# Optimization experiments

Hardware: AMD Instinct MI355X
Metric: run time of the kernel (lower is better)

## Reference

```python
import jax, jax.numpy as jnp
import numpy as np

EMBED_DIM = 1024
NUM_HEADS = 16
HEAD_DIM = EMBED_DIM // NUM_HEADS
N, S = 4, 8192


def setup_inputs() -> dict:
    key = jax.random.key(0)
    ks = jax.random.split(key, 9)
    sc = 1.0 / np.sqrt(EMBED_DIM)
    d = {"x": jax.random.normal(ks[0], (N, S, EMBED_DIM), dtype=jnp.float32)}
    for i, name in enumerate(["Wq", "Wk", "Wv", "Wo"]):
        d[name] = jax.random.normal(ks[1 + i], (EMBED_DIM, EMBED_DIM), dtype=jnp.float32) * sc
    for i, name in enumerate(["bq", "bk", "bv", "bo"]):
        d[name] = jax.random.normal(ks[5 + i], (EMBED_DIM,), dtype=jnp.float32) * 0.01
    return d


def reference(x, Wq, Wk, Wv, Wo, bq, bk, bv, bo):
    n, s, e = x.shape
    # projections: nn.Linear => x @ W.T + b
    Q = x @ Wq.T + bq
    K = x @ Wk.T + bk
    V = x @ Wv.T + bv
    # (N, S, H, D) -> (N, H, S, D), matching torch .view().transpose(1, 2)
    Q = Q.reshape(n, s, NUM_HEADS, HEAD_DIM).transpose(0, 2, 1, 3)
    K = K.reshape(n, s, NUM_HEADS, HEAD_DIM).transpose(0, 2, 1, 3)
    V = V.reshape(n, s, NUM_HEADS, HEAD_DIM).transpose(0, 2, 1, 3)
    # Faithful to the original (buggy) einsum labeling: on (N,H,S,D) tensors
    # 'nqhd,nkhd->nhqk' attends OVER THE HEAD AXIS -> energy (N, S, H, H)
    energy = jnp.einsum('nqhd,nkhd->nhqk', Q, K)
    attention = jax.nn.softmax(energy / jnp.sqrt(jnp.float32(e)), axis=3)
    # out: (N, H, S, D), then reshaped as if (N, S, H*D) — exact original math
    out = jnp.einsum('nhql,nlhd->nqhd', attention, V).reshape(n, s, e)
    return out @ Wo.T + bo
```

## Files before the change

### kernel.cpp

```cpp
#include <hip/hip_runtime.h>
#include <cstdint>
#include <cstddef>

typedef unsigned short u16;
typedef __attribute__((ext_vector_type(8))) __bf16 bf16x8;
typedef __attribute__((ext_vector_type(4))) float floatx4;

typedef const __attribute__((address_space(1))) void* gptr_t;
typedef __attribute__((address_space(3))) void* lptr_t;

__device__ __forceinline__ u16 f2b(float f) {
    unsigned u = __builtin_bit_cast(unsigned, f);
    u += 0x7fffu + ((u >> 16) & 1u);
    return (u16)(u >> 16);
}

template <int N>
__device__ __forceinline__ float ror_add(float x) {
    int y = __builtin_amdgcn_update_dpp(0, __builtin_bit_cast(int, x), 0x120 + N, 0xF, 0xF, true);
    return x + __builtin_bit_cast(float, y);
}
template <int N>
__device__ __forceinline__ float ror_max(float x) {
    int y = __builtin_amdgcn_update_dpp(0, __builtin_bit_cast(int, x), 0x120 + N, 0xF, 0xF, true);
    return fmaxf(x, __builtin_bit_cast(float, y));
}

__global__ void cast_x(const float* __restrict__ in, u16* __restrict__ out, int n4) {
    const int stride = gridDim.x * blockDim.x;
    for (int i = blockIdx.x * blockDim.x + threadIdx.x; i < n4; i += stride) {
        const float4 v = ((const float4*)in)[i];
        ushort4 o;
        o.x = f2b(v.x); o.y = f2b(v.y); o.z = f2b(v.z); o.w = f2b(v.w);
        ((ushort4*)out)[i] = o;
    }
}

__global__ void cast_w(const float* __restrict__ Wq, const float* __restrict__ Wk,
                       const float* __restrict__ Wv, const float* __restrict__ Wo,
                       u16* __restrict__ Wqkv, u16* __restrict__ Wob) {
    const int stride = gridDim.x * blockDim.x;
    for (int i = blockIdx.x * blockDim.x + threadIdx.x; i < 1048576; i += stride) {
        const int which = i >> 18;
        const int local = i & 0x3FFFF;
        const float* src = which == 0 ? Wq : which == 1 ? Wk : which == 2 ? Wv : Wo;
        const float4 v = ((const float4*)src)[local];
        ushort4 o;
        o.x = f2b(v.x); o.y = f2b(v.y); o.z = f2b(v.z); o.w = f2b(v.w);
        ushort4* dst = which < 3 ? (ushort4*)Wqkv + which * 262144 + local
                                 : (ushort4*)Wob + local;
        *dst = o;
    }
}


#define MFMA16(va, vb, vc) __builtin_amdgcn_mfma_f32_16x16x32_bf16((va), (vb), (vc), 0, 0, 0)
#define PH_BAR()  __builtin_amdgcn_s_barrier()
#define PH_LGKM() asm volatile("s_waitcnt lgkmcnt(0)" ::: "memory")

template <bool OUT_BF16>
__global__ __launch_bounds__(512, 2)
void gemm8(const u16* __restrict__ A, const u16* __restrict__ B,
           const float* __restrict__ b0, const float* __restrict__ b1,
           const float* __restrict__ b2, void* __restrict__ Cout,
           int N, int mshift)
{
    __shared__ __align__(16) u16 lds[65536];

    const int nwg = gridDim.x;
    const int bid = blockIdx.x;
    const int swz = (bid & 7) * (nwg >> 3) + (bid >> 3);
    const int ntile = swz >> mshift;
    const int mtile = swz & ((1 << mshift) - 1);
    const int bm0 = mtile << 8;
    const int bn0 = ntile << 8;

    const int tid  = threadIdx.x;
    const int lane = tid & 63;
    const int wv   = tid >> 6;
    const int wm   = wv >> 2;
    const int wn   = wv & 3;
    const int lrow = lane & 15;
    const int quad = lane >> 4;

    const int srow = lane >> 2;
    const int scol = ((lane & 3) * 8) ^ (((lane >> 5) & 1) << 4);
    const u16* aS = A + (size_t)(bm0 + wv * 16 + srow) * 1024 + scol;
    const u16* bS = B + (size_t)(bn0 + wv * 16 + srow) * 1024 + scol;
    u16* aD = lds +         wv * 1024 + lane * 8;
    u16* bD = lds + 32768 + wv * 1024 + lane * 8;

    const int laneSw = lrow * 32 + ((quad * 8) ^ ((lrow >> 3) << 4));
    const u16* pA = lds +         wm * 8192 + laneSw;
    const u16* pB = lds + 32768 + wn * 4096 + laneSw;

    auto stage = [&](const u16* src, u16* dst, int kt, int half, int buf) {
        const u16* s = src + (size_t)half * 131072 + kt * 64;
        u16* d = dst + buf * 16384 + half * 8192;
        __builtin_amdgcn_global_load_lds((gptr_t)s,        (lptr_t)d,         16, 0, 0);
        __builtin_amdgcn_global_load_lds((gptr_t)(s + 32), (lptr_t)(d + 512), 16, 0, 0);
    };

    stage(aS, aD, 0, 0, 0);
    stage(aS, aD, 0, 1, 0);
    stage(bS, bD, 0, 0, 0);
    stage(bS, bD, 0, 1, 0);
    asm volatile("" ::: "memory");
    stage(bS, bD, 1, 0, 1);
    stage(bS, bD, 1, 1, 1);
    asm volatile("s_waitcnt vmcnt(4)" ::: "memory");
    PH_BAR();

    const floatx4 fz = {0.f, 0.f, 0.f, 0.f};
    floatx4 acc[8][4];
    #pragma unroll
    for (int i = 0; i < 8; ++i)
        #pragma unroll
        for (int t = 0; t < 4; ++t) acc[i][t] = fz;

    bf16x8 a[4][2], p0[2][2], p1[2][2];

    for (int j = 0; j < 8; ++j) {
        const int kt1 = 2 * j + 1;
        const int kt2 = 2 * j + 2;
        const int kt3 = 2 * j + 3;
        const bool more = (j < 7);

        #pragma unroll
        for (int i = 0; i < 4; ++i) {
            a[i][0] = *(const bf16x8*)(pA + i * 1024);
            a[i][1] = *(const bf16x8*)(pA + i * 1024 + 512);
        }
        #pragma unroll
        for (int t = 0; t < 2; ++t) {
            p0[t][0] = *(const bf16x8*)(pB + t * 1024);
            p0[t][1] = *(const bf16x8*)(pB + t * 1024 + 512);
        }
        stage(aS, aD, kt1, 0, 1);
        PH_BAR(); PH_LGKM();
        __builtin_amdgcn_s_setprio(1);
        #pragma unroll
        for (int i = 0; i < 4; ++i)
            #pragma unroll
            for (int t = 0; t < 2; ++t) {
                acc[i][t] = MFMA16(a[i][0], p0[t][0], acc[i][t]);
                acc[i][t] = MFMA16(a[i][1], p0[t][1], acc[i][t]);
            }
        __builtin_amdgcn_s_setprio(0);
        PH_BAR();

        #pragma unroll
        for (int t = 0; t < 2; ++t) {
            p1[t][0] = *(const bf16x8*)(pB + 2048 + t * 1024);
            p1[t][1] = *(const bf16x8*)(pB + 2048 + t * 1024 + 512);
        }
        stage(aS, aD, kt1, 1, 1);
        PH_BAR(); PH_LGKM();
        __builtin_amdgcn_s_setprio(1);
        #pragma unroll
        for (int i = 0; i < 4; ++i)
            #pragma unroll
            for (int t = 0; t < 2; ++t) {
                acc[i][2 + t] = MFMA16(a[i][0], p1[t][0], acc[i][2 + t]);
                acc[i][2 + t] = MFMA16(a[i][1], p1[t][1], acc[i][2 + t]);
            }
        __builtin_amdgcn_s_setprio(0);
        PH_BAR();

        #pragma unroll
        for (int i = 0; i < 4; ++i) {
            a[i][0] = *(const bf16x8*)(pA + 4096 + i * 1024);
            a[i][1] = *(const bf16x8*)(pA + 4096 + i * 1024 + 512);
        }
        if (more) stage(bS, bD, kt2, 0, 0);
        PH_BAR(); PH_LGKM();
        __builtin_amdgcn_s_setprio(1);
        #pragma unroll
        for (int i = 0; i < 4; ++i)
            #pragma unroll
            for (int t = 0; t < 2; ++t) {
                acc[4 + i][2 + t] = MFMA16(a[i][0], p1[t][0], acc[4 + i][2 + t]);
                acc[4 + i][2 + t] = MFMA16(a[i][1], p1[t][1], acc[4 + i][2 + t]);
            }
        __builtin_amdgcn_s_setprio(0);
        PH_BAR();

        if (more) stage(bS, bD, kt2, 1, 0);
        PH_BAR();
        __builtin_amdgcn_s_setprio(1);
        #pragma unroll
        for (int i = 0; i < 4; ++i)
            #pragma unroll
            for (int t = 0; t < 2; ++t) {
                acc[4 + i][t] = MFMA16(a[i][0], p0[t][0], acc[4 + i][t]);
                acc[4 + i][t] = MFMA16(a[i][1], p0[t][1], acc[4 + i][t]);
            }
        __builtin_amdgcn_s_setprio(0);
        if (more) asm volatile("s_waitcnt vmcnt(4)" ::: "memory");
        else      asm volatile("s_waitcnt vmcnt(0)" ::: "memory");
        PH_BAR();

        #pragma unroll
        for (int i = 0; i < 4; ++i) {
            a[i][0] = *(const bf16x8*)(pA + 16384 + i * 1024);
            a[i][1] = *(const bf16x8*)(pA + 16384 + i * 1024 + 512);
        }
        #pragma unroll
        for (int t = 0; t < 2; ++t) {
            p0[t][0] = *(const bf16x8*)(pB + 16384 + t * 1024);
            p0[t][1] = *(const bf16x8*)(pB + 16384 + t * 1024 + 512);
        }
        if (more) stage(aS, aD, kt2, 0, 0);
        PH_BAR(); PH_LGKM();
        __builtin_amdgcn_s_setprio(1);
        #pragma unroll
        for (int i = 0; i < 4; ++i)
            #pragma unroll
            for (int t = 0; t < 2; ++t) {
                acc[i][t] = MFMA16(a[i][0], p0[t][0], acc[i][t]);
                acc[i][t] = MFMA16(a[i][1], p0[t][1], acc[i][t]);
            }
        __builtin_amdgcn_s_setprio(0);
        PH_BAR();

        #pragma unroll
        for (int t = 0; t < 2; ++t) {
            p1[t][0] = *(const bf16x8*)(pB + 16384 + 2048 + t * 1024);
            p1[t][1] = *(const bf16x8*)(pB + 16384 + 2048 + t * 1024 + 512);
        }
        if (more) stage(aS, aD, kt2, 1, 0);
        PH_BAR(); PH_LGKM();
        __builtin_amdgcn_s_setprio(1);
        #pragma unroll
        for (int i = 0; i < 4; ++i)
            #pragma unroll
            for (int t = 0; t < 2; ++t) {
                acc[i][2 + t] = MFMA16(a[i][0], p1[t][0], acc[i][2 + t]);
                acc[i][2 + t] = MFMA16(a[i][1], p1[t][1], acc[i][2 + t]);
            }
        __builtin_amdgcn_s_setprio(0);
        PH_BAR();

        #pragma unroll
        for (int i = 0; i < 4; ++i) {
            a[i][0] = *(const bf16x8*)(pA + 16384 + 4096 + i * 1024);
            a[i][1] = *(const bf16x8*)(pA + 16384 + 4096 + i * 1024 + 512);
        }
        if (more) stage(bS, bD, kt3, 0, 1);
        PH_BAR(); PH_LGKM();
        __builtin_amdgcn_s_setprio(1);
        #pragma unroll
        for (int i = 0; i < 4; ++i)
            #pragma unroll
            for (int t = 0; t < 2; ++t) {
                acc[4 + i][2 + t] = MFMA16(a[i][0], p1[t][0], acc[4 + i][2 + t]);
                acc[4 + i][2 + t] = MFMA16(a[i][1], p1[t][1], acc[4 + i][2 + t]);
            }
        __builtin_amdgcn_s_setprio(0);
        PH_BAR();

        if (more) stage(bS, bD, kt3, 1, 1);
        PH_BAR();
        __builtin_amdgcn_s_setprio(1);
        #pragma unroll
        for (int i = 0; i < 4; ++i)
            #pragma unroll
            for (int t = 0; t < 2; ++t) {
                acc[4 + i][t] = MFMA16(a[i][0], p0[t][0], acc[4 + i][t]);
                acc[4 + i][t] = MFMA16(a[i][1], p0[t][1], acc[4 + i][t]);
            }
        __builtin_amdgcn_s_setprio(0);
        asm volatile("s_waitcnt vmcnt(4)" ::: "memory");
        PH_BAR();
    }

    float bsv[4];
    #pragma unroll
    for (int t = 0; t < 4; ++t) {
        const int n = bn0 + wn * 64 + t * 16 + lrow;
        const float* bp = n < 1024 ? b0 : (n < 2048 ? b1 : b2);
        bsv[t] = bp[n & 1023];
    }
    #pragma unroll
    for (int i = 0; i < 8; ++i) {
        const int mbase = bm0 + wm * 128 + i * 16 + quad * 4;
        #pragma unroll
        for (int t = 0; t < 4; ++t) {
            const int n = bn0 + wn * 64 + t * 16 + lrow;
            #pragma unroll
            for (int r = 0; r < 4; ++r) {
                const float v = acc[i][t][r] + bsv[t];
                const size_t idx = (size_t)(mbase + r) * N + n;
                if constexpr (OUT_BF16) ((u16*)Cout)[idx] = f2b(v);
                else                    ((float*)Cout)[idx] = v;
            }
        }
    }
}

__global__ __launch_bounds__(256)
void attn_v3(const u16* __restrict__ QKV, u16* __restrict__ Z)
{
    __shared__ __align__(16) u16 sV[4][1024];
    __shared__ __align__(16) u16 sA[4][640];
    __shared__ __align__(16) u16 sY[16 * 1152];

    const int tid  = threadIdx.x;
    const int lane = tid & 63;
    const int wv   = tid >> 6;
    const int lrow = lane & 15;
    const int quad = lane >> 4;
    const int pp   = lane >> 3;
    const int cc   = lane & 7;

    #pragma unroll
    for (int i = 0; i < 4; i++) {
        const int idx = i * 64 + lane;
        sA[wv][(idx >> 4) * 40 + 16 + (idx & 15)] = 0;
    }

    const int tgrp = blockIdx.x * 16;
    const int nb   = tgrp >> 13;
    const int sg   = (tgrp & 8191) >> 4;

    const floatx4 fzero = {0.f, 0.f, 0.f, 0.f};

    for (int tt = 0; tt < 4; tt++) {
        const int t = wv * 4 + tt;
        const u16* base = QKV + (size_t)(tgrp + t) * 3072;

        const bf16x8 q0 = *(const bf16x8*)(base + lrow * 64      + quad * 8);
        const bf16x8 q1 = *(const bf16x8*)(base + lrow * 64 + 32 + quad * 8);
        const bf16x8 k0 = *(const bf16x8*)(base + 1024 + lrow * 64      + quad * 8);
        const bf16x8 k1 = *(const bf16x8*)(base + 1024 + lrow * 64 + 32 + quad * 8);

        const u16* V = base + 2048;
        const bf16x8 va = *(const bf16x8*)(V + (2 * pp)     * 64 + cc * 8);
        const bf16x8 vb = *(const bf16x8*)(V + (2 * pp + 1) * 64 + cc * 8);
        #pragma unroll
        for (int s = 0; s < 8; s++) {
            const unsigned pv = (unsigned)__builtin_bit_cast(u16, (__bf16)va[s]) |
                                ((unsigned)__builtin_bit_cast(u16, (__bf16)vb[s]) << 16);
            *(unsigned*)&sV[wv][(s * 8 + cc) * 16 + 2 * pp] = pv;
        }

        floatx4 e = fzero;
        e = __builtin_amdgcn_mfma_f32_16x16x32_bf16(q0, k0, e, 0, 0, 0);
        e = __builtin_amdgcn_mfma_f32_16x16x32_bf16(q1, k1, e, 0, 0, 0);

        #pragma unroll
        for (int r = 0; r < 4; r++) {
            const float xv = e[r] * 0.03125f;
            float mx = xv;
            mx = ror_max<1>(mx); mx = ror_max<2>(mx);
            mx = ror_max<4>(mx); mx = ror_max<8>(mx);
            const float p = __expf(xv - mx);
            float s = p;
            s = ror_add<1>(s); s = ror_add<2>(s);
            s = ror_add<4>(s); s = ror_add<8>(s);
            sA[wv][(quad * 4 + r) * 40 + lrow] = f2b(p * __builtin_amdgcn_rcpf(s));
        }

        const bf16x8 af = *(const bf16x8*)&sA[wv][lrow * 40 + quad * 8];

        bf16x8 bfr[4];
        #pragma unroll
        for (int j = 0; j < 4; j++)
            #pragma unroll
            for (int jj = 0; jj < 8; jj++)
                bfr[j][jj] = __builtin_bit_cast(__bf16, (u16)0);
        if (quad < 2) {
            #pragma unroll
            for (int j = 0; j < 4; j++) {
                const int pr = (lrow & 7) * 8 + j * 2 + (lrow >> 3);
                bfr[j] = *(const bf16x8*)&sV[wv][pr * 16 + quad * 8];
            }
        }

        #pragma unroll
        for (int j = 0; j < 4; j++) {
            const floatx4 y = __builtin_amdgcn_mfma_f32_16x16x32_bf16(af, bfr[j], fzero, 0, 0, 0);
            #pragma unroll
            for (int r = 0; r < 4; r++)
                sY[t * 1152 + (quad * 4 + r) * 72 + j * 16 + lrow] = f2b(y[r]);
        }
    }

    __syncthreads();

    const int h   = tid >> 4;
    const int pos = tid & 15;
    u16* zrow = Z + (size_t)(nb * 8192 + h * 512 + sg) * 1024;
    #pragma unroll
    for (int it = 0; it < 8; it++) {
        const int c16 = it * 16 + pos;
        const int t = c16 >> 3, dc = c16 & 7;
        const uint4 v = *(const uint4*)&sY[t * 1152 + h * 72 + dc * 8];
        *(uint4*)(zrow + c16 * 8) = v;
    }
}

extern "C" void kernel_launch(void* const* d_in, const int* in_sizes, int n_in,
                              void* d_out, int out_size, void* d_ws, size_t ws_size,
                              hipStream_t stream)
{
    (void)in_sizes; (void)n_in; (void)out_size;
    const float* x  = (const float*)d_in[0];
    const float* Wq = (const float*)d_in[1];
    const float* Wk = (const float*)d_in[2];
    const float* Wv = (const float*)d_in[3];
    const float* Wo = (const float*)d_in[4];
    const float* bq = (const float*)d_in[5];
    const float* bk = (const float*)d_in[6];
    const float* bv = (const float*)d_in[7];
    const float* bo = (const float*)d_in[8];

    const size_t Mtot = 32768;
    char* ws = (char*)d_ws;
    u16* Xbf  = (u16*)ws;
    u16* Wqkv = (u16*)(ws + (64ull << 20));
    u16* Wob  = (u16*)(ws + (64ull << 20) + (6ull << 20));
    char* dyn = ws + (72ull << 20);
    const size_t fixed = (72ull << 20);

    int c = 4;
    for (int cc = 1; cc <= 4; cc <<= 1) {
        size_t Rr = Mtot / cc;
        if (fixed + Rr * 3072 * 2 + Rr * 1024 * 2 <= ws_size) { c = cc; break; }
    }
    const size_t R = Mtot / c;
    u16* QKV = (u16*)dyn;
    u16* Zb  = (u16*)(dyn + R * 3072 * 2);

    cast_x<<<dim3(4096), dim3(256), 0, stream>>>(x, Xbf, (int)(Mtot * 1024 / 4));
    cast_w<<<dim3(1024), dim3(256), 0, stream>>>(Wq, Wk, Wv, Wo, Wqkv, Wob);

    const int mt  = (int)(R >> 8);
    const int msh = __builtin_ctz((unsigned)mt);

    for (int ci = 0; ci < c; ci++) {
        const u16* Ab   = Xbf + (size_t)ci * R * 1024;
        float*     outp = (float*)d_out + (size_t)ci * R * 1024;
        gemm8<true><<<dim3(mt * 12), dim3(512), 0, stream>>>(Ab, Wqkv, bq, bk, bv, QKV, 3072, msh);
        attn_v3<<<dim3((unsigned)(R / 16)), dim3(256), 0, stream>>>(QKV, Zb);
        gemm8<false><<<dim3(mt * 4), dim3(512), 0, stream>>>(Zb, Wob, bo, bo, bo, outp, 1024, msh);
    }
}
```

Before: 573.3 us.

## Restructure GEMM main loop with double-buffered register fragments and sched barriers

Rewrites the bf16 GEMM inner loop so LDS fragment reads for the next MFMA block are issued before the current block's MFMAs, using separate even/odd register sets. It drops the explicit lgkmcnt(0) waits, stages whole A/B k-tiles at once, and adds sched_barrier fences with vmcnt waits at new points. The aim is to hide LDS read latency and cut barrier stalls between MFMA phases, at the cost of more VGPR pressure. Correctness now depends on the reworked buffer and wait-count accounting.

```diff
diff --git a/kernel.cpp b/kernel.cpp
--- a/kernel.cpp
+++ b/kernel.cpp
@@ -56,7 +56,19 @@
 
 #define MFMA16(va, vb, vc) __builtin_amdgcn_mfma_f32_16x16x32_bf16((va), (vb), (vc), 0, 0, 0)
 #define PH_BAR()  __builtin_amdgcn_s_barrier()
-#define PH_LGKM() asm volatile("s_waitcnt lgkmcnt(0)" ::: "memory")
+#define SB0()     __builtin_amdgcn_sched_barrier(0)
+#define VM4()     asm volatile("s_waitcnt vmcnt(4)" ::: "memory")
+#define VM0()     asm volatile("s_waitcnt vmcnt(0)" ::: "memory")
+
+#define MMA_BLK(af, bf, MI, TJ)                                                        \
+    _Pragma("unroll")                                                                  \
+    for (int i_ = 0; i_ < 4; ++i_) {                                                   \
+        _Pragma("unroll")                                                              \
+        for (int t_ = 0; t_ < 2; ++t_) {                                               \
+            acc[(MI)+i_][(TJ)+t_] = MFMA16(af[i_][0], bf[t_][0], acc[(MI)+i_][(TJ)+t_]); \
+            acc[(MI)+i_][(TJ)+t_] = MFMA16(af[i_][1], bf[t_][1], acc[(MI)+i_][(TJ)+t_]); \
+        }                                                                              \
+    }
 
 template <bool OUT_BF16>
 __global__ __launch_bounds__(512, 2)
@@ -94,22 +106,40 @@
     const u16* pA = lds +         wm * 8192 + laneSw;
     const u16* pB = lds + 32768 + wn * 4096 + laneSw;
 
-    auto stage = [&](const u16* src, u16* dst, int kt, int half, int buf) {
-        const u16* s = src + (size_t)half * 131072 + kt * 64;
-        u16* d = dst + buf * 16384 + half * 8192;
-        __builtin_amdgcn_global_load_lds((gptr_t)s,        (lptr_t)d,         16, 0, 0);
-        __builtin_amdgcn_global_load_lds((gptr_t)(s + 32), (lptr_t)(d + 512), 16, 0, 0);
+    auto stage2 = [&](const u16* src, u16* dst, int kt) {
+        #pragma unroll
+        for (int h = 0; h < 2; ++h) {
+            const u16* s = src + (size_t)h * 131072 + kt * 64;
+            u16* d = dst + h * 8192;
+            __builtin_amdgcn_global_load_lds((gptr_t)s,        (lptr_t)d,         16, 0, 0);
+            __builtin_amdgcn_global_load_lds((gptr_t)(s + 32), (lptr_t)(d + 512), 16, 0, 0);
+        }
     };
 
-    stage(aS, aD, 0, 0, 0);
-    stage(aS, aD, 0, 1, 0);
-    stage(bS, bD, 0, 0, 0);
-    stage(bS, bD, 0, 1, 0);
+    bf16x8 aE[4][2], aO[4][2], p1[2][2], p0E[2][2], p0O[2][2];
+
+    auto readA = [&](bf16x8 (&d)[4][2], int off) {
+        #pragma unroll
+        for (int i = 0; i < 4; ++i) {
+            d[i][0] = *(const bf16x8*)(pA + off + i * 1024);
+            d[i][1] = *(const bf16x8*)(pA + off + i * 1024 + 512);
+        }
+    };
+    auto readB = [&](bf16x8 (&d)[2][2], int off) {
+        #pragma unroll
+        for (int t = 0; t < 2; ++t) {
+            d[t][0] = *(const bf16x8*)(pB + off + t * 1024);
+            d[t][1] = *(const bf16x8*)(pB + off + t * 1024 + 512);
+        }
+    };
+
+    stage2(bS, bD, 0);
+    stage2(aS, aD, 0);
     asm volatile("" ::: "memory");
-    stage(bS, bD, 1, 0, 1);
-    stage(bS, bD, 1, 1, 1);
-    asm volatile("s_waitcnt vmcnt(4)" ::: "memory");
-    PH_BAR();
+    stage2(bS, bD + 16384, 1);
+    stage2(aS, aD + 16384, 1);
+    asm volatile("s_waitcnt vmcnt(8)" ::: "memory");
+    PH_BAR(); SB0();
 
     const floatx4 fz = {0.f, 0.f, 0.f, 0.f};
     floatx4 acc[8][4];
@@ -118,160 +148,81 @@
         #pragma unroll
         for (int t = 0; t < 4; ++t) acc[i][t] = fz;
 
-    bf16x8 a[4][2], p0[2][2], p1[2][2];
+    readA(aE, 0);
+    readB(p0E, 0);
 
     for (int j = 0; j < 8; ++j) {
-        const int kt1 = 2 * j + 1;
+        const bool more = (j < 7);
         const int kt2 = 2 * j + 2;
         const int kt3 = 2 * j + 3;
-        const bool more = (j < 7);
-
-        #pragma unroll
-        for (int i = 0; i < 4; ++i) {
-            a[i][0] = *(const bf16x8*)(pA + i * 1024);
-            a[i][1] = *(const bf16x8*)(pA + i * 1024 + 512);
-        }
-        #pragma unroll
-        for (int t = 0; t < 2; ++t) {
-            p0[t][0] = *(const bf16x8*)(pB + t * 1024);
-            p0[t][1] = *(const bf16x8*)(pB + t * 1024 + 512);
-        }
-        stage(aS, aD, kt1, 0, 1);
-        PH_BAR(); PH_LGKM();
-        __builtin_amdgcn_s_setprio(1);
-        #pragma unroll
-        for (int i = 0; i < 4; ++i)
-            #pragma unroll
-            for (int t = 0; t < 2; ++t) {
-                acc[i][t] = MFMA16(a[i][0], p0[t][0], acc[i][t]);
-                acc[i][t] = MFMA16(a[i][1], p0[t][1], acc[i][t]);
-            }
-        __builtin_amdgcn_s_setprio(0);
-        PH_BAR();
-
-        #pragma unroll
-        for (int t = 0; t < 2; ++t) {
-            p1[t][0] = *(const bf16x8*)(pB + 2048 + t * 1024);
-            p1[t][1] = *(const bf16x8*)(pB + 2048 + t * 1024 + 512);
-        }
-        stage(aS, aD, kt1, 1, 1);
-        PH_BAR(); PH_LGKM();
-        __builtin_amdgcn_s_setprio(1);
-        #pragma unroll
-        for (int i = 0; i < 4; ++i)
-            #pragma unroll
-            for (int t = 0; t < 2; ++t) {
-                acc[i][2 + t] = MFMA16(a[i][0], p1[t][0], acc[i][2 + t]);
-                acc[i][2 + t] = MFMA16(a[i][1], p1[t][1], acc[i][2 + t]);
-            }
-        __builtin_amdgcn_s_setprio(0);
-        PH_BAR();
-
-        #pragma unroll
-        for (int i = 0; i < 4; ++i) {
-            a[i][0] = *(const bf16x8*)(pA + 4096 + i * 1024);
-            a[i][1] = *(const bf16x8*)(pA + 4096 + i * 1024 + 512);
-        }
-        if (more) stage(bS, bD, kt2, 0, 0);
-        PH_BAR(); PH_LGKM();
-        __builtin_amdgcn_s_setprio(1);
-        #pragma unroll
-        for (int i = 0; i < 4; ++i)
-            #pragma unroll
-            for (int t = 0; t < 2; ++t) {
-                acc[4 + i][2 + t] = MFMA16(a[i][0], p1[t][0], acc[4 + i][2 + t]);
-                acc[4 + i][2 + t] = MFMA16(a[i][1], p1[t][1], acc[4 + i][2 + t]);
-            }
-        __builtin_amdgcn_s_setprio(0);
-        PH_BAR();
-
-        if (more) stage(bS, bD, kt2, 1, 0);
-        PH_BAR();
-        __builtin_amdgcn_s_setprio(1);
-        #pragma unroll
-        for (int i = 0; i < 4; ++i)
-            #pragma unroll
-            for (int t = 0; t < 2; ++t) {
-                acc[4 + i][t] = MFMA16(a[i][0], p0[t][0], acc[4 + i][t]);
-                acc[4 + i][t] = MFMA16(a[i][1], p0[t][1], acc[4 + i][t]);
-            }
-        __builtin_amdgcn_s_setprio(0);
-        if (more) asm volatile("s_waitcnt vmcnt(4)" ::: "memory");
-        else      asm volatile("s_waitcnt vmcnt(0)" ::: "memory");
-        PH_BAR();
-
-        #pragma unroll
-        for (int i = 0; i < 4; ++i) {
-            a[i][0] = *(const bf16x8*)(pA + 16384 + i * 1024);
-            a[i][1] = *(const bf16x8*)(pA + 16384 + i * 1024 + 512);
-        }
-        #pragma unroll
-        for (int t = 0; t < 2; ++t) {
-            p0[t][0] = *(const bf16x8*)(pB + 16384 + t * 1024);
-            p0[t][1] = *(const bf16x8*)(pB + 16384 + t * 1024 + 512);
-        }
-        if (more) stage(aS, aD, kt2, 0, 0);
-        PH_BAR(); PH_LGKM();
-        __builtin_amdgcn_s_setprio(1);
-        #pragma unroll
-        for (int i = 0; i < 4; ++i)
-            #pragma unroll
-            for (int t = 0; t < 2; ++t) {
-                acc[i][t] = MFMA16(a[i][0], p0[t][0], acc[i][t]);
-                acc[i][t] = MFMA16(a[i][1], p0[t][1], acc[i][t]);
-            }
-        __builtin_amdgcn_s_setprio(0);
-        PH_BAR();
-
-        #pragma unroll
-        for (int t = 0; t < 2; ++t) {
-            p1[t][0] = *(const bf16x8*)(pB + 16384 + 2048 + t * 1024);
-            p1[t][1] = *(const bf16x8*)(pB + 16384 + 2048 + t * 1024 + 512);
-        }
-        if (more) stage(aS, aD, kt2, 1, 0);
-        PH_BAR(); PH_LGKM();
-        __builtin_amdgcn_s_setprio(1);
-        #pragma unroll
-        for (int i = 0; i < 4; ++i)
-            #pragma unroll
-            for (int t = 0; t < 2; ++t) {
-                acc[i][2 + t] = MFMA16(a[i][0], p1[t][0], acc[i][2 + t]);
-                acc[i][2 + t] = MFMA16(a[i][1], p1[t][1], acc[i][2 + t]);
-            }
-        __builtin_amdgcn_s_setprio(0);
-        PH_BAR();
-
-        #pragma unroll
-        for (int i = 0; i < 4; ++i) {
-            a[i][0] = *(const bf16x8*)(pA + 16384 + 4096 + i * 1024);
-            a[i][1] = *(const bf16x8*)(pA + 16384 + 4096 + i * 1024 + 512);
-        }
-        if (more) stage(bS, bD, kt3, 0, 1);
-        PH_BAR(); PH_LGKM();
-        __builtin_amdgcn_s_setprio(1);
-        #pragma unroll
-        for (int i = 0; i < 4; ++i)
-            #pragma unroll
-            for (int t = 0; t < 2; ++t) {
-                acc[4 + i][2 + t] = MFMA16(a[i][0], p1[t][0], acc[4 + i][2 + t]);
-                acc[4 + i][2 + t] = MFMA16(a[i][1], p1[t][1], acc[4 + i][2 + t]);
-            }
-        __builtin_amdgcn_s_setprio(0);
-        PH_BAR();
-
-        if (more) stage(bS, bD, kt3, 1, 1);
-        PH_BAR();
-        __builtin_amdgcn_s_setprio(1);
-        #pragma unroll
-        for (int i = 0; i < 4; ++i)
-            #pragma unroll
-            for (int t = 0; t < 2; ++t) {
-                acc[4 + i][t] = MFMA16(a[i][0], p0[t][0], acc[4 + i][t]);
-                acc[4 + i][t] = MFMA16(a[i][1], p0[t][1], acc[4 + i][t]);
-            }
-        __builtin_amdgcn_s_setprio(0);
-        asm volatile("s_waitcnt vmcnt(4)" ::: "memory");
-        PH_BAR();
+
+        readB(p1, 2048);
+        SB0();
+        __builtin_amdgcn_s_setprio(1);
+        MMA_BLK(aE, p0E, 0, 0);
+        __builtin_amdgcn_s_setprio(0);
+        PH_BAR(); SB0();
+
+        readA(aO, 4096);
+        SB0();
+        __builtin_amdgcn_s_setprio(1);
+        MMA_BLK(aE, p1, 0, 2);
+        __builtin_amdgcn_s_setprio(0);
+        VM4();
+        PH_BAR(); SB0();
+
+        if (more) stage2(bS, bD, kt2);
+        readB(p0O, 16384);
+        SB0();
+        __builtin_amdgcn_s_setprio(1);
+        MMA_BLK(aO, p1, 4, 2);
+        __builtin_amdgcn_s_setprio(0);
+        if (more) { VM4(); } else { VM0(); }
+        PH_BAR(); SB0();
+
+        if (more) stage2(aS, aD, kt2);
+        readA(aE, 16384);
+        SB0();
+        __builtin_amdgcn_s_setprio(1);
+        MMA_BLK(aO, p0E, 4, 0);
+        __builtin_amdgcn_s_setprio(0);
+        PH_BAR(); SB0();
+
+        readB(p1, 16384 + 2048);
+        SB0();
+        __builtin_amdgcn_s_setprio(1);
+        MMA_BLK(aE, p0O, 0, 0);
+        __builtin_amdgcn_s_setprio(0);
+        PH_BAR(); SB0();
+
+        readA(aO, 16384 + 4096);
+        SB0();
+        __builtin_amdgcn_s_setprio(1);
+        MMA_BLK(aE, p1, 0, 2);
+        __builtin_amdgcn_s_setprio(0);
+        if (more) VM4();
+        PH_BAR(); SB0();
+
+        if (more) {
+            stage2(bS, bD + 16384, kt3);
+            readB(p0E, 0);
+        }
+        SB0();
+        __builtin_amdgcn_s_setprio(1);
+        MMA_BLK(aO, p1, 4, 2);
+        __builtin_amdgcn_s_setprio(0);
+        if (more) VM4();
+        PH_BAR(); SB0();
+
+        if (more) {
+            stage2(aS, aD + 16384, kt3);
+            readA(aE, 0);
+        }
+        SB0();
+        __builtin_amdgcn_s_setprio(1);
+        MMA_BLK(aO, p0O, 4, 0);
+        __builtin_amdgcn_s_setprio(0);
+        PH_BAR(); SB0();
     }
 
     float bsv[4];
```

Measured after the change: 618.8 us. 1.08x slower.
